# Kernel tuning notes

Measured on AMD Instinct MI355X. Metric: run time of the kernel, lower is better.

## Reference

```python
import jax, jax.numpy as jnp
import numpy as np

WS = 6      # window_size
SS = 3      # shift_size
NH = 8      # num_heads
DIM = 384
HD = DIM // NH
SCALE = HD ** -0.5


def _window_mask(H, W):
    # region ids: [:ss,:ss]=0, [:ss,ss:]=1, [ss:,:ss]=2, [ss:,ss:]=3
    row = (jnp.arange(H) >= SS).astype(jnp.int32)
    col = (jnp.arange(W) >= SS).astype(jnp.int32)
    region = row[:, None] * 2 + col[None, :]            # (H, W)
    region = jnp.roll(region, (-SS, -SS), axis=(0, 1))
    ids = region.reshape(H // WS, WS, W // WS, WS).transpose(0, 2, 1, 3)
    ids = ids.reshape(-1, WS * WS)                      # (nW, V)
    eq = ids[:, :, None] == ids[:, None, :]             # (nW, V, V)
    return jnp.where(eq, 0.0, -jnp.inf).astype(jnp.float32)


def setup_inputs():
    key = jax.random.key(0)
    k = jax.random.split(key, 5)
    B, H, W, D = 32, 48, 48, DIM
    return {
        "x": jax.random.normal(k[0], (B, H, W, D), jnp.float32),
        "w_qkv": jax.random.normal(k[1], (D, 3 * D), jnp.float32) * 0.02,
        "b_qkv": jax.random.normal(k[2], (3 * D,), jnp.float32) * 0.02,
        "w_proj": jax.random.normal(k[3], (D, D), jnp.float32) * 0.02,
        "b_proj": jax.random.normal(k[4], (D,), jnp.float32) * 0.02,
    }


def reference(x, w_qkv, b_qkv, w_proj, b_proj):
    B, H, W, D = x.shape
    nWh, nWw = H // WS, W // WS
    nW, V = nWh * nWw, WS * WS

    x = jnp.roll(x, (-SS, -SS), axis=(1, 2))
    amask = _window_mask(H, W)                          # (nW, V, V)

    # window partition -> (B*nW, V, D)
    xw = x.reshape(B, nWh, WS, nWw, WS, D).transpose(0, 1, 3, 2, 4, 5)
    xw = xw.reshape(B * nW, V, D)

    qkv = xw @ w_qkv + b_qkv                            # (M, V, 3D)
    qkv = qkv.reshape(B * nW, V, 3, NH, HD).transpose(2, 0, 3, 1, 4)
    q, k, v = qkv[0], qkv[1], qkv[2]                    # (M, NH, V, HD)

    scores = jnp.einsum("mhvd,mhud->mhvu", q, k) * SCALE
    scores = scores.reshape(B, nW, NH, V, V) + amask[None, :, None]
    attn = jax.nn.softmax(scores, axis=-1).reshape(B * nW, NH, V, V)

    out = jnp.einsum("mhvu,mhud->mhvd", attn, v)        # (M, NH, V, HD)
    out = out.transpose(0, 2, 1, 3).reshape(B * nW, V, D)

    # window reverse -> (B, H, W, D)
    out = out.reshape(B, nWh, nWw, WS, WS, D).transpose(0, 1, 3, 2, 4, 5)
    out = out.reshape(B, H, W, D)
    out = jnp.roll(out, (SS, SS), axis=(1, 2))
    return out @ w_proj + b_proj
```

## Files before the change

kernel.cpp:

```cpp
#include <hip/hip_runtime.h>
#include <hip/hip_bf16.h>

namespace {

constexpr int Bn   = 32;
constexpr int IMG  = 48;
constexpr int Dm   = 384;
constexpr int NHn  = 8;
constexpr int WSn  = 6;
constexpr int NWn  = 64;
constexpr int Mn   = Bn * NWn;
constexpr int Vn   = 36;
constexpr int ROWS = Mn * Vn;
constexpr int K3   = 3 * Dm;
constexpr int HEADS_E = Vn * 48;
constexpr float SCALE = 0.14433756729740643f;

using short8 = __attribute__((ext_vector_type(8))) short;
using f32x4  = __attribute__((ext_vector_type(4))) float;

__device__ __forceinline__ float bf2f(unsigned short u) {
    return __uint_as_float(((unsigned)u) << 16);
}
__device__ __forceinline__ unsigned short f2bf(float f) {
    unsigned u = __float_as_uint(f);
    u += 0x7FFFu + ((u >> 16) & 1u);
    return (unsigned short)(u >> 16);
}

__device__ __forceinline__ int invol(int f) {
    return (f & 56) | ((f ^ (f >> 3)) & 7);
}

__device__ __forceinline__ void gl_lds16(const unsigned short* g, unsigned short* l) {
    __builtin_amdgcn_global_load_lds(
        (const __attribute__((address_space(1))) unsigned int*)g,
        (__attribute__((address_space(3))) unsigned int*)l, 16, 0, 0);
}

__device__ __forceinline__ int gather_base(int row) {
    int m = row / Vn, v = row - m * Vn;
    int b = m >> 6, w = m & 63;
    int wh = w >> 3, ww = w & 7;
    int gh = wh * WSn + v / WSn;
    int gw = ww * WSn + v % WSn;
    int fi = (gh + 3) % IMG;
    int fj = (gw + 3) % IMG;
    return ((b * IMG + fi) * IMG + fj) * Dm;
}

__device__ __forceinline__ int region_id(int t, int wh, int ww) {
    int hi = (wh == 7) ? ((t / 6) < 3) : 1;
    int lo = (ww == 7) ? ((t % 6) < 3) : 1;
    return (hi << 1) | lo;
}

__global__ __launch_bounds__(256)
void gather_x(const float* __restrict__ x, unsigned short* __restrict__ xg)
{
    int idx = blockIdx.x * 256 + threadIdx.x;
    int row = idx / 96;
    int c4  = (idx - row * 96) * 4;
    float4 v = *(const float4*)(x + (size_t)gather_base(row) + c4);
    ushort4 o;
    o.x = f2bf(v.x); o.y = f2bf(v.y); o.z = f2bf(v.z); o.w = f2bf(v.w);
    *(ushort4*)(xg + (size_t)row * Dm + c4) = o;
}

__global__ __launch_bounds__(256)
void prep_w(const float* __restrict__ wq, const float* __restrict__ wp,
            unsigned short* __restrict__ wqT, unsigned short* __restrict__ wpT)
{
    int idx = blockIdx.x * 256 + threadIdx.x;
    if (idx < K3 * Dm) {
        int n = idx / Dm, k = idx - n * Dm;
        wqT[idx] = f2bf(wq[(size_t)k * K3 + n]);
    } else {
        int i2 = idx - K3 * Dm;
        if (i2 < Dm * Dm) {
            int n = i2 / Dm, k = i2 - n * Dm;
            wpT[i2] = f2bf(wp[(size_t)k * Dm + n]);
        }
    }
}

__global__ __launch_bounds__(256)
void qkv_mfma(const unsigned short* __restrict__ xg,
              const unsigned short* __restrict__ wqT,
              const float* __restrict__ bq,
              unsigned short* __restrict__ qh,
              unsigned short* __restrict__ kh,
              unsigned short* __restrict__ vh)
{
    __shared__ __align__(16) unsigned short As[2][128 * 32];
    __shared__ __align__(16) unsigned short Bs[2][128 * 32];

    const int tid  = threadIdx.x;
    const int wave = tid >> 6, lane = tid & 63;
    const int quad = lane >> 4, l15 = lane & 15;
    const int id = (blockIdx.x & 7) * 648 + (blockIdx.x >> 3);
    const int nT = id % (K3 / 128);
    const int mT = id / (K3 / 128);
    const int rowA0 = mT * 128, rowB0 = nT * 128;

    const int fS  = invol(lane);
    const int rS  = fS >> 2;
    const int kcS = (fS & 3) * 8;
    const unsigned short* gA = xg  + (size_t)(rowA0 + wave * 32 + rS) * Dm + kcS;
    const unsigned short* gB = wqT + (size_t)(rowB0 + wave * 32 + rS) * Dm + kcS;

    const int wm = wave >> 1, wn = wave & 1;
    int aoff[4], boff[4];
#pragma unroll
    for (int i = 0; i < 4; i++) {
        int R = wm * 64 + i * 16 + l15;
        aoff[i] = (R >> 4) * 512 + invol((R & 15) * 4 + quad) * 8;
        int S = wn * 64 + i * 16 + l15;
        boff[i] = (S >> 4) * 512 + invol((S & 15) * 4 + quad) * 8;
    }

    auto STAGE = [&](int buf, int k0) {
        gl_lds16(gA + k0,           &As[buf][(wave * 32) * 32]);
        gl_lds16(gA + 16 * Dm + k0, &As[buf][(wave * 32 + 16) * 32]);
        gl_lds16(gB + k0,           &Bs[buf][(wave * 32) * 32]);
        gl_lds16(gB + 16 * Dm + k0, &Bs[buf][(wave * 32 + 16) * 32]);
    };

    f32x4 acc[4][4];
#pragma unroll
    for (int i = 0; i < 4; i++)
#pragma unroll
        for (int j = 0; j < 4; j++) acc[i][j] = (f32x4){0.f, 0.f, 0.f, 0.f};

    STAGE(0, 0);
    __syncthreads();

    for (int k0 = 0; k0 < Dm; k0 += 32) {
        const int cur = (k0 >> 5) & 1;
        if (k0 + 32 < Dm) STAGE(cur ^ 1, k0 + 32);
        short8 af[4], bfr[4];
#pragma unroll
        for (int i = 0; i < 4; i++) af[i]  = *(const short8*)&As[cur][aoff[i]];
#pragma unroll
        for (int j = 0; j < 4; j++) bfr[j] = *(const short8*)&Bs[cur][boff[j]];
#pragma unroll
        for (int i = 0; i < 4; i++)
#pragma unroll
            for (int j = 0; j < 4; j++)
                acc[i][j] = __builtin_amdgcn_mfma_f32_16x16x32_bf16(af[i], bfr[j], acc[i][j], 0, 0, 0);
        if (k0 + 32 < Dm) __syncthreads();
    }

    unsigned short* outb = (nT < 3) ? qh : (nT < 6) ? kh : vh;
    const int csub = (nT < 3) ? 0 : (nT < 6) ? 384 : 768;
#pragma unroll
    for (int j = 0; j < 4; j++) {
        int col = rowB0 + wn * 64 + j * 16 + l15;
        float b = bq[col];
        int c  = col - csub;
        int hh = c / 48, dd = c - hh * 48;
#pragma unroll
        for (int i = 0; i < 4; i++) {
#pragma unroll
            for (int r = 0; r < 4; r++) {
                int row = rowA0 + wm * 64 + i * 16 + quad * 4 + r;
                int mm = row / 36, vv = row - mm * 36;
                outb[((size_t)(mm * 8 + hh) * 36 + vv) * 48 + dd] = f2bf(acc[i][j][r] + b);
            }
        }
    }
}

__global__ __launch_bounds__(256)
void attn_mfma(const unsigned short* __restrict__ qh,
               const unsigned short* __restrict__ kh,
               const unsigned short* __restrict__ vh,
               unsigned short* __restrict__ att)
{
    __shared__ __align__(16) unsigned short Pl[4][48 * 56];
    __shared__ __align__(16) unsigned short Vt[4][48 * 64];

    const int tid  = threadIdx.x;
    const int wave = tid >> 6, lane = tid & 63;
    const int quad = lane >> 4, l15 = lane & 15;
    const int W = blockIdx.x * 4 + wave;
    const int m = W >> 3, h = W & 7;
    const int w = m & 63, wh = w >> 3, ww = w & 7;
    const bool need_mask = (wh == 7) || (ww == 7);

    const short8 zf = {0, 0, 0, 0, 0, 0, 0, 0};

    {
        short8* vz = (short8*)&Vt[0][0];
#pragma unroll
        for (int z = 0; z < 6; z++) vz[z * 256 + tid] = zf;
    }
    __syncthreads();

    const size_t hb = (size_t)(m * 8 + h) * HEADS_E;

    const unsigned short* qb = qh + hb;
    const unsigned short* kb = kh + hb;
    short8 qf[3][2], kf[3][2];
#pragma unroll
    for (int t = 0; t < 3; t++) {
        const unsigned short* qr = qb + (t * 16 + l15) * 48;
        qf[t][0] = *(const short8*)(qr + quad * 8);
        qf[t][1] = (quad < 2) ? *(const short8*)(qr + 32 + quad * 8) : zf;
        const unsigned short* kr = kb + (t * 16 + l15) * 48;
        kf[t][0] = *(const short8*)(kr + quad * 8);
        kf[t][1] = *(const short8*)(kr + 32 + quad * 8);
    }

    unsigned short* vws = &Vt[wave][0];
    {
        const unsigned short* vb = vh + hb;
#pragma unroll
        for (int p = 0; p < 4; p++) {
            int c = p * 64 + lane;
            if (c < 216) {
                short8 vv = *(const short8*)(vb + c * 8);
                int v  = c / 6, d0 = (c - v * 6) * 8;
                int g  = v >> 3, v7 = v & 7;
#pragma unroll
                for (int jj = 0; jj < 8; jj++) {
                    int d = d0 + jj;
                    int slot = (g + (d & 7) + (d >> 3)) & 7;
                    vws[d * 64 + slot * 8 + v7] = (unsigned short)vv[jj];
                }
            }
        }
    }

    f32x4 acc[3][3];
#pragma unroll
    for (int i = 0; i < 3; i++)
#pragma unroll
        for (int j = 0; j < 3; j++) acc[i][j] = (f32x4){0.f, 0.f, 0.f, 0.f};
    __builtin_amdgcn_s_setprio(1);
#pragma unroll
    for (int i = 0; i < 3; i++)
#pragma unroll
        for (int j = 0; j < 3; j++) {
            acc[i][j] = __builtin_amdgcn_mfma_f32_16x16x32_bf16(qf[i][0], kf[j][0], acc[i][j], 0, 0, 0);
            acc[i][j] = __builtin_amdgcn_mfma_f32_16x16x32_bf16(qf[i][1], kf[j][1], acc[i][j], 0, 0, 0);
        }
    __builtin_amdgcn_s_setprio(0);

#pragma unroll
    for (int i = 0; i < 3; i++) {
        float rs[4] = {0.f, 0.f, 0.f, 0.f};
        if (need_mask) {
#pragma unroll
            for (int j = 0; j < 3; j++) {
                int C = j * 16 + l15;
                int idc = region_id(C, wh, ww);
#pragma unroll
                for (int r = 0; r < 4; r++) {
                    int R = i * 16 + quad * 4 + r;
                    int idr = region_id(R, wh, ww);
                    float s = acc[i][j][r] * SCALE;
                    s = (C >= 36 || idr != idc) ? -1e30f : fminf(s, 30.f);
                    float e = __expf(s);
                    acc[i][j][r] = e;
                    rs[r] += e;
                }
            }
        } else {
#pragma unroll
            for (int j = 0; j < 3; j++) {
                int C = j * 16 + l15;
#pragma unroll
                for (int r = 0; r < 4; r++) {
                    float s = acc[i][j][r] * SCALE;
                    s = (C >= 36) ? -1e30f : fminf(s, 30.f);
                    float e = __expf(s);
                    acc[i][j][r] = e;
                    rs[r] += e;
                }
            }
        }
#pragma unroll
        for (int r = 0; r < 4; r++) {
#pragma unroll
            for (int d = 1; d < 16; d <<= 1) rs[r] += __shfl_xor(rs[r], d, 16);
            rs[r] = 1.f / rs[r];
        }
#pragma unroll
        for (int j = 0; j < 3; j++)
#pragma unroll
            for (int r = 0; r < 4; r++) {
                int R = i * 16 + quad * 4 + r;
                int C = j * 16 + l15;
                Pl[wave][R * 56 + C] = f2bf(acc[i][j][r] * rs[r]);
            }
    }
    __syncthreads();

    short8 pf[3][2], vf[3][2];
#pragma unroll
    for (int t = 0; t < 3; t++) {
        const unsigned short* pr = &Pl[wave][(t * 16 + l15) * 56];
        pf[t][0] = *(const short8*)(pr + quad * 8);
        pf[t][1] = (quad < 2) ? *(const short8*)(pr + 32 + quad * 8) : zf;
        int d  = t * 16 + l15;
        int sb = (d & 7) + (d >> 3);
        vf[t][0] = *(const short8*)(vws + d * 64 + (((quad + sb) & 7) * 8));
        vf[t][1] = *(const short8*)(vws + d * 64 + (((quad + 4 + sb) & 7) * 8));
    }
    f32x4 oacc[3][3];
#pragma unroll
    for (int i = 0; i < 3; i++)
#pragma unroll
        for (int j = 0; j < 3; j++) oacc[i][j] = (f32x4){0.f, 0.f, 0.f, 0.f};
    __builtin_amdgcn_s_setprio(1);
#pragma unroll
    for (int i = 0; i < 3; i++)
#pragma unroll
        for (int j = 0; j < 3; j++) {
            oacc[i][j] = __builtin_amdgcn_mfma_f32_16x16x32_bf16(pf[i][0], vf[j][0], oacc[i][j], 0, 0, 0);
            oacc[i][j] = __builtin_amdgcn_mfma_f32_16x16x32_bf16(pf[i][1], vf[j][1], oacc[i][j], 0, 0, 0);
        }
    __builtin_amdgcn_s_setprio(0);

#pragma unroll
    for (int i = 0; i < 3; i++)
#pragma unroll
        for (int r = 0; r < 4; r++) {
            int R = i * 16 + quad * 4 + r;
            if (R < 36) {
#pragma unroll
                for (int j = 0; j < 3; j++)
                    att[((size_t)m * 36 + R) * Dm + h * 48 + j * 16 + l15] = f2bf(oacc[i][j][r]);
            }
        }
}

__global__ __launch_bounds__(256)
void proj_mfma(const unsigned short* __restrict__ att,
               const unsigned short* __restrict__ wpT,
               const float* __restrict__ bp,
               float* __restrict__ out)
{
    __shared__ __align__(16) unsigned short As[2][128 * 32];
    __shared__ __align__(16) unsigned short Bs[2][128 * 32];
    __shared__ int rowOut[128];

    const int tid  = threadIdx.x;
    const int wave = tid >> 6, lane = tid & 63;
    const int quad = lane >> 4, l15 = lane & 15;
    const int id = (blockIdx.x & 7) * 216 + (blockIdx.x >> 3);
    const int nT = id % (Dm / 128);
    const int mT = id / (Dm / 128);
    const int rowA0 = mT * 128, rowB0 = nT * 128;

    if (tid < 128) rowOut[tid] = gather_base(rowA0 + tid);

    const int fS  = invol(lane);
    const int rS  = fS >> 2;
    const int kcS = (fS & 3) * 8;
    const unsigned short* gA = att + (size_t)(rowA0 + wave * 32 + rS) * Dm + kcS;
    const unsigned short* gB = wpT + (size_t)(rowB0 + wave * 32 + rS) * Dm + kcS;

    const int wm = wave >> 1, wn = wave & 1;
    int aoff[4], boff[4];
#pragma unroll
    for (int i = 0; i < 4; i++) {
        int R = wm * 64 + i * 16 + l15;
        aoff[i] = (R >> 4) * 512 + invol((R & 15) * 4 + quad) * 8;
        int S = wn * 64 + i * 16 + l15;
        boff[i] = (S >> 4) * 512 + invol((S & 15) * 4 + quad) * 8;
    }

    auto STAGE = [&](int buf, int k0) {
        gl_lds16(gA + k0,           &As[buf][(wave * 32) * 32]);
        gl_lds16(gA + 16 * Dm + k0, &As[buf][(wave * 32 + 16) * 32]);
        gl_lds16(gB + k0,           &Bs[buf][(wave * 32) * 32]);
        gl_lds16(gB + 16 * Dm + k0, &Bs[buf][(wave * 32 + 16) * 32]);
    };

    f32x4 acc[4][4];
#pragma unroll
    for (int i = 0; i < 4; i++)
#pragma unroll
        for (int j = 0; j < 4; j++) acc[i][j] = (f32x4){0.f, 0.f, 0.f, 0.f};

    STAGE(0, 0);
    __syncthreads();

    for (int k0 = 0; k0 < Dm; k0 += 32) {
        const int cur = (k0 >> 5) & 1;
        if (k0 + 32 < Dm) STAGE(cur ^ 1, k0 + 32);
        short8 af[4], bfr[4];
#pragma unroll
        for (int i = 0; i < 4; i++) af[i]  = *(const short8*)&As[cur][aoff[i]];
#pragma unroll
        for (int j = 0; j < 4; j++) bfr[j] = *(const short8*)&Bs[cur][boff[j]];
#pragma unroll
        for (int i = 0; i < 4; i++)
#pragma unroll
            for (int j = 0; j < 4; j++)
                acc[i][j] = __builtin_amdgcn_mfma_f32_16x16x32_bf16(af[i], bfr[j], acc[i][j], 0, 0, 0);
        if (k0 + 32 < Dm) __syncthreads();
    }

#pragma unroll
    for (int j = 0; j < 4; j++) {
        int col = rowB0 + wn * 64 + j * 16 + l15;
        float b = bp[col];
#pragma unroll
        for (int i = 0; i < 4; i++) {
#pragma unroll
            for (int r = 0; r < 4; r++) {
                int lrow = wm * 64 + i * 16 + quad * 4 + r;
                out[(size_t)rowOut[lrow] + col] = acc[i][j][r] + b;
            }
        }
    }
}

}

extern "C" void kernel_launch(void* const* d_in, const int* in_sizes, int n_in,
                              void* d_out, int out_size, void* d_ws, size_t ws_size,
                              hipStream_t stream)
{
    const float* x  = (const float*)d_in[0];
    const float* wq = (const float*)d_in[1];
    const float* bq = (const float*)d_in[2];
    const float* wp = (const float*)d_in[3];
    const float* bp = (const float*)d_in[4];
    float* out = (float*)d_out;

    const size_t HE   = (size_t)Mn * NHn * HEADS_E;
    const size_t XG_E = (size_t)ROWS * Dm;
    unsigned short* qh  = (unsigned short*)d_ws;
    unsigned short* kh  = qh + HE;
    unsigned short* vh  = kh + HE;
    unsigned short* xg  = vh + HE;
    unsigned short* att = xg;
    unsigned short* wqT = xg + XG_E;
    unsigned short* wpT = wqT + (size_t)K3 * Dm;

    prep_w   <<<(K3 * Dm + Dm * Dm + 255) / 256, 256, 0, stream>>>(wq, wp, wqT, wpT);
    gather_x <<<ROWS * (Dm / 4) / 256,            256, 0, stream>>>(x, xg);
    qkv_mfma <<<(ROWS / 128) * (K3 / 128),        256, 0, stream>>>(xg, wqT, bq, qh, kh, vh);
    attn_mfma<<<(Mn * NHn) / 4,                   256, 0, stream>>>(qh, kh, vh, att);
    proj_mfma<<<(ROWS / 128) * (Dm / 128),        256, 0, stream>>>(att, wpT, bp, out);
}
```

Measured before the change: 421.3 us.

## Triple-buffer LDS staging in QKV and projection GEMMs with vmcnt-gated barriers

Both MFMA GEMM kernels move from double-buffered LDS with full __syncthreads to a three-stage ring buffer. Two tiles are prefetched ahead, and each step waits only until the oldest outstanding direct-to-LDS loads complete (vmcnt(4)) before a raw s_barrier. The K loop is fully unrolled. The aim is to keep two global loads in flight while MFMA runs, hiding memory latency. In exchange LDS use grows from 32KB to 48KB per block, which may lower occupancy.

```diff
diff --git a/kernel.cpp b/kernel.cpp
--- a/kernel.cpp
+++ b/kernel.cpp
@@ -92,8 +92,8 @@
               unsigned short* __restrict__ kh,
               unsigned short* __restrict__ vh)
 {
-    __shared__ __align__(16) unsigned short As[2][128 * 32];
-    __shared__ __align__(16) unsigned short Bs[2][128 * 32];
+    __shared__ __align__(16) unsigned short As[3][128 * 32];
+    __shared__ __align__(16) unsigned short Bs[3][128 * 32];
 
     const int tid  = threadIdx.x;
     const int wave = tid >> 6, lane = tid & 63;
@@ -119,37 +119,46 @@
         boff[i] = (S >> 4) * 512 + invol((S & 15) * 4 + quad) * 8;
     }
 
+    f32x4 acc[4][4];
+#pragma unroll
+    for (int i = 0; i < 4; i++)
+#pragma unroll
+        for (int j = 0; j < 4; j++) acc[i][j] = (f32x4){0.f, 0.f, 0.f, 0.f};
+
     auto STAGE = [&](int buf, int k0) {
         gl_lds16(gA + k0,           &As[buf][(wave * 32) * 32]);
         gl_lds16(gA + 16 * Dm + k0, &As[buf][(wave * 32 + 16) * 32]);
         gl_lds16(gB + k0,           &Bs[buf][(wave * 32) * 32]);
         gl_lds16(gB + 16 * Dm + k0, &Bs[buf][(wave * 32 + 16) * 32]);
     };
-
-    f32x4 acc[4][4];
-#pragma unroll
-    for (int i = 0; i < 4; i++)
-#pragma unroll
-        for (int j = 0; j < 4; j++) acc[i][j] = (f32x4){0.f, 0.f, 0.f, 0.f};
-
-    STAGE(0, 0);
-    __syncthreads();
-
-    for (int k0 = 0; k0 < Dm; k0 += 32) {
-        const int cur = (k0 >> 5) & 1;
-        if (k0 + 32 < Dm) STAGE(cur ^ 1, k0 + 32);
+    auto COMPUTE = [&](int buf) {
         short8 af[4], bfr[4];
 #pragma unroll
-        for (int i = 0; i < 4; i++) af[i]  = *(const short8*)&As[cur][aoff[i]];
-#pragma unroll
-        for (int j = 0; j < 4; j++) bfr[j] = *(const short8*)&Bs[cur][boff[j]];
+        for (int i = 0; i < 4; i++) af[i]  = *(const short8*)&As[buf][aoff[i]];
+#pragma unroll
+        for (int j = 0; j < 4; j++) bfr[j] = *(const short8*)&Bs[buf][boff[j]];
 #pragma unroll
         for (int i = 0; i < 4; i++)
 #pragma unroll
             for (int j = 0; j < 4; j++)
                 acc[i][j] = __builtin_amdgcn_mfma_f32_16x16x32_bf16(af[i], bfr[j], acc[i][j], 0, 0, 0);
-        if (k0 + 32 < Dm) __syncthreads();
-    }
+    };
+
+    STAGE(0, 0);
+    STAGE(1, 32);
+#pragma unroll
+    for (int t = 0; t < 10; ++t) {
+        asm volatile("s_waitcnt vmcnt(4)" ::: "memory");
+        __builtin_amdgcn_s_barrier();
+        STAGE((t + 2) % 3, (t + 2) * 32);
+        COMPUTE(t % 3);
+    }
+    asm volatile("s_waitcnt vmcnt(4)" ::: "memory");
+    __builtin_amdgcn_s_barrier();
+    COMPUTE(10 % 3);
+    asm volatile("s_waitcnt vmcnt(0)" ::: "memory");
+    __builtin_amdgcn_s_barrier();
+    COMPUTE(11 % 3);
 
     unsigned short* outb = (nT < 3) ? qh : (nT < 6) ? kh : vh;
     const int csub = (nT < 3) ? 0 : (nT < 6) ? 384 : 768;
@@ -342,8 +351,8 @@
                const float* __restrict__ bp,
                float* __restrict__ out)
 {
-    __shared__ __align__(16) unsigned short As[2][128 * 32];
-    __shared__ __align__(16) unsigned short Bs[2][128 * 32];
+    __shared__ __align__(16) unsigned short As[3][128 * 32];
+    __shared__ __align__(16) unsigned short Bs[3][128 * 32];
     __shared__ int rowOut[128];
 
     const int tid  = threadIdx.x;
@@ -372,37 +381,46 @@
         boff[i] = (S >> 4) * 512 + invol((S & 15) * 4 + quad) * 8;
     }
 
+    f32x4 acc[4][4];
+#pragma unroll
+    for (int i = 0; i < 4; i++)
+#pragma unroll
+        for (int j = 0; j < 4; j++) acc[i][j] = (f32x4){0.f, 0.f, 0.f, 0.f};
+
     auto STAGE = [&](int buf, int k0) {
         gl_lds16(gA + k0,           &As[buf][(wave * 32) * 32]);
         gl_lds16(gA + 16 * Dm + k0, &As[buf][(wave * 32 + 16) * 32]);
         gl_lds16(gB + k0,           &Bs[buf][(wave * 32) * 32]);
         gl_lds16(gB + 16 * Dm + k0, &Bs[buf][(wave * 32 + 16) * 32]);
     };
-
-    f32x4 acc[4][4];
-#pragma unroll
-    for (int i = 0; i < 4; i++)
-#pragma unroll
-        for (int j = 0; j < 4; j++) acc[i][j] = (f32x4){0.f, 0.f, 0.f, 0.f};
-
-    STAGE(0, 0);
-    __syncthreads();
-
-    for (int k0 = 0; k0 < Dm; k0 += 32) {
-        const int cur = (k0 >> 5) & 1;
-        if (k0 + 32 < Dm) STAGE(cur ^ 1, k0 + 32);
+    auto COMPUTE = [&](int buf) {
         short8 af[4], bfr[4];
 #pragma unroll
-        for (int i = 0; i < 4; i++) af[i]  = *(const short8*)&As[cur][aoff[i]];
-#pragma unroll
-        for (int j = 0; j < 4; j++) bfr[j] = *(const short8*)&Bs[cur][boff[j]];
+        for (int i = 0; i < 4; i++) af[i]  = *(const short8*)&As[buf][aoff[i]];
+#pragma unroll
+        for (int j = 0; j < 4; j++) bfr[j] = *(const short8*)&Bs[buf][boff[j]];
 #pragma unroll
         for (int i = 0; i < 4; i++)
 #pragma unroll
             for (int j = 0; j < 4; j++)
                 acc[i][j] = __builtin_amdgcn_mfma_f32_16x16x32_bf16(af[i], bfr[j], acc[i][j], 0, 0, 0);
-        if (k0 + 32 < Dm) __syncthreads();
-    }
+    };
+
+    STAGE(0, 0);
+    STAGE(1, 32);
+#pragma unroll
+    for (int t = 0; t < 10; ++t) {
+        asm volatile("s_waitcnt vmcnt(4)" ::: "memory");
+        __builtin_amdgcn_s_barrier();
+        STAGE((t + 2) % 3, (t + 2) * 32);
+        COMPUTE(t % 3);
+    }
+    asm volatile("s_waitcnt vmcnt(4)" ::: "memory");
+    __builtin_amdgcn_s_barrier();
+    COMPUTE(10 % 3);
+    asm volatile("s_waitcnt vmcnt(0)" ::: "memory");
+    __builtin_amdgcn_s_barrier();
+    COMPUTE(11 % 3);
 
 #pragma unroll
     for (int j = 0; j < 4; j++) {
```

Result: no change. 422.2 us (+0.2%).
